# Optimization experiments

Hardware: AMD Instinct MI355X
Metric: run time of the kernel (lower is better)

The kernel has to match this reference:

```python
import jax, jax.numpy as jnp
import numpy as np

NPOINT = 1024
NSAMPLE = 32
RADIUS = 0.2


def index_points2(points, idx):
    # points: (B,N,D), idx: (B,S) -> (B,S,D)
    return jnp.take_along_axis(points, idx[..., None], axis=1)


def index_points3(points, idx):
    # points: (B,N,D), idx: (B,S,K) -> (B,S,K,D)
    B, S, K = idx.shape
    flat = jnp.take_along_axis(points, idx.reshape(B, S * K)[..., None], axis=1)
    return flat.reshape(B, S, K, points.shape[-1])


def farthest_point_sampling(xyz, npoint):
    # xyz: (B,N,3) -> (B,npoint) int32 indices. First point deterministic (index 0).
    B, N, _ = xyz.shape
    first = jnp.zeros((B,), jnp.int32)
    chosen = jnp.zeros((B, npoint), jnp.int32).at[:, 0].set(first)
    first_xyz = index_points2(xyz, first[:, None])[:, 0, :]
    dist_min = jnp.sum((xyz - first_xyz[:, None, :]) ** 2, axis=-1)  # (B,N)

    def body(i, carry):
        chosen, dist_min = carry
        far = jnp.argmax(dist_min, axis=-1).astype(jnp.int32)  # (B,)
        far_xyz = index_points2(xyz, far[:, None])[:, 0, :]
        d = jnp.sum((xyz - far_xyz[:, None, :]) ** 2, axis=-1)
        return chosen.at[:, i].set(far), jnp.minimum(dist_min, d)

    chosen, _ = jax.lax.fori_loop(1, npoint, body, (chosen, dist_min))
    return chosen


def query_ball_point(radius, nsample, xyz, new_xyz):
    # (B,S,N) squared distances; out-of-ball -> inf; take nsample nearest (stable argsort).
    dist = jnp.sum((new_xyz[:, :, None, :] - xyz[:, None, :, :]) ** 2, axis=-1)
    dist_m = jnp.where(dist <= radius ** 2, dist, jnp.inf)
    return jnp.argsort(dist_m, axis=-1)[:, :, :nsample]


def mlp2(x, Wa, ba, Wb, bb, act2):
    h = jax.nn.relu(x @ Wa + ba)
    return act2(h @ Wb + bb)


def reference(xyz, features, W1, b1, W2, b2, W3, b3, W4, b4):
    fps_idx = farthest_point_sampling(xyz, NPOINT)          # (B,S)
    new_xyz = index_points2(xyz, fps_idx)                   # (B,S,3)
    group_idx = query_ball_point(RADIUS, NSAMPLE, xyz, new_xyz)  # (B,S,K)
    grouped_xyz = index_points3(xyz, group_idx)             # (B,S,K,3)
    grouped_xyz_norm = grouped_xyz - new_xyz[:, :, None, :]
    grouped_feats = index_points3(features, group_idx)      # (B,S,K,C)
    f_in = jnp.concatenate([grouped_xyz_norm, grouped_feats], axis=-1)
    f_prime = mlp2(f_in, W1, b1, W2, b2, jax.nn.relu)       # (B,S,K,H)
    f_mean = jnp.mean(f_prime, axis=2, keepdims=True)
    w_in = jnp.concatenate([grouped_xyz_norm, f_prime - f_mean], axis=-1)
    alpha = mlp2(w_in, W3, b3, W4, b4, jax.nn.sigmoid)      # (B,S,K,H)
    f_out = jnp.sum(alpha * f_prime, axis=2)                # (B,S,H)
    return new_xyz, f_out


def setup_inputs() -> dict:
    key = jax.random.key(0)
    ks = jax.random.split(key, 8)
    B, N, C, H = 16, 4096, 64, 128
    xyz = jax.random.uniform(ks[0], (B, N, 3), dtype=jnp.float32)
    features = jax.random.normal(ks[1], (B, N, C), dtype=jnp.float32)
    s = 0.1
    return {
        "xyz": xyz,
        "features": features,
        "W1": jax.random.normal(ks[2], (3 + C, H), dtype=jnp.float32) * s,
        "b1": jnp.zeros((H,), jnp.float32),
        "W2": jax.random.normal(ks[3], (H, H), dtype=jnp.float32) * s,
        "b2": jnp.zeros((H,), jnp.float32),
        "W3": jax.random.normal(ks[4], (3 + H, H), dtype=jnp.float32) * s,
        "b3": jnp.zeros((H,), jnp.float32),
        "W4": jax.random.normal(ks[5], (H, H), dtype=jnp.float32) * s,
        "b4": jnp.zeros((H,), jnp.float32),
    }
```

## Files before the change

### kernel.cpp

```cpp
#include <hip/hip_runtime.h>

typedef unsigned short u16;
typedef unsigned int   u32;
typedef unsigned long long u64;
typedef short s8v __attribute__((ext_vector_type(8)));
typedef float f4v __attribute__((ext_vector_type(4)));
typedef float f2v __attribute__((ext_vector_type(2)));
typedef unsigned long long ull2 __attribute__((ext_vector_type(2)));

#define STRIDE 168
#define CAP 256
#define OFF_G1 0
#define OFF_G2 12288
#define OFF_G3 28672
#define OFF_G4 49152

__device__ __forceinline__ float bf2f(u16 u){ return __uint_as_float(((u32)u)<<16); }
__device__ __forceinline__ u16 f2bf(float f){
  u32 u = __float_as_uint(f);
  return (u16)((u + 0x7FFFu + ((u>>16)&1u)) >> 16);
}
__device__ __forceinline__ float sqd(float ax,float ay,float az,float bx,float by,float bz){
  float dx=ax-bx, dy=ay-by, dz=az-bz;
  return __fadd_rn(__fadd_rn(__fmul_rn(dx,dx),__fmul_rn(dy,dy)),__fmul_rn(dz,dz));
}

#define WMAX_STEP(v, CTRL) { \
  u32 _t = (u32)__builtin_amdgcn_update_dpp(0, (int)(v), CTRL, 0xf, 0xf, false); \
  (v) = (v) > _t ? (v) : _t; }
#define QMAX64(k, CTRL) { \
  u32 _lo=(u32)(k), _hi=(u32)((k)>>32); \
  u32 _plo=(u32)__builtin_amdgcn_update_dpp(0,(int)_lo,CTRL,0xf,0xf,true); \
  u32 _phi=(u32)__builtin_amdgcn_update_dpp(0,(int)_hi,CTRL,0xf,0xf,true); \
  u64 _o=((u64)_phi<<32)|_plo; (k) = (k)>_o ? (k) : _o; }

__global__ __launch_bounds__(512) void fps_kernel(const float* __restrict__ xyz,
                                                  float* __restrict__ newxyz){
  __shared__ __align__(16) float S[4096*3];
  __shared__ __align__(16) float R[1024*3];
  __shared__ u64 red[2][8];
  const int b = blockIdx.x, tid = threadIdx.x;
  const int lane = tid & 63, wv = tid >> 6;
  const float* xb = xyz + (size_t)b*4096*3;
  #pragma unroll
  for(int j=0;j<6;j++) ((float4*)S)[j*512+tid] = ((const float4*)xb)[j*512+tid];
  __syncthreads();
  f2v X[4],Y[4],Z[4],DM[4];
  const float x0=S[0], y0=S[1], z0=S[2];
  {
    #pragma clang fp contract(off)
    const f2v fx2={x0,x0}, fy2={y0,y0}, fz2={z0,z0};
    #pragma unroll
    for(int k2=0;k2<4;k2++){
      int p0 = tid*8 + 2*k2;
      X[k2] = (f2v){S[p0*3],   S[p0*3+3]};
      Y[k2] = (f2v){S[p0*3+1], S[p0*3+4]};
      Z[k2] = (f2v){S[p0*3+2], S[p0*3+5]};
      f2v dx=X[k2]-fx2, dy=Y[k2]-fy2, dz=Z[k2]-fz2;
      DM[k2] = (dx*dx + dy*dy) + dz*dz;
    }
  }
  if(tid==0){ R[0]=x0; R[1]=y0; R[2]=z0; }
  for(int i=1;i<1024;i++){
    f2v a = __builtin_elementwise_max(DM[0],DM[1]);
    f2v c = __builtin_elementwise_max(DM[2],DM[3]);
    f2v mm = __builtin_elementwise_max(a,c);
    float vm = fmaxf(mm[0], mm[1]);
    u32 m8 = 0;
    #pragma unroll
    for(int j=0;j<8;j++) m8 |= (DM[j>>1][j&1]==vm) ? (1u<<j) : 0u;
    int jm = __ffs(m8)-1;
    u32 w = __float_as_uint(vm);
    WMAX_STEP(w, 0x111); WMAX_STEP(w, 0x112); WMAX_STEP(w, 0x114);
    WMAX_STEP(w, 0x118); WMAX_STEP(w, 0x142); WMAX_STEP(w, 0x143);
    u32 wm = (u32)__builtin_amdgcn_readlane((int)w, 63);
    u64 msk = __ballot(__float_as_uint(vm) == wm);
    int ldr = __ffsll((unsigned long long)msk) - 1;
    int pj  = __builtin_amdgcn_readlane(jm, ldr);
    int p   = (wv*64 + ldr)*8 + pj;
    if(lane==0) red[i&1][wv] = ((u64)wm<<32) | (u32)(~(u32)p);
    __syncthreads();
    u64 k = red[i&1][lane&7];
    QMAX64(k, 0x121); QMAX64(k, 0x122); QMAX64(k, 0x124);
    int far = (int)(~(u32)k) & 4095;
    float fx=S[far*3], fy=S[far*3+1], fz=S[far*3+2];
    if(tid==0){ R[i*3]=fx; R[i*3+1]=fy; R[i*3+2]=fz; }
    {
      #pragma clang fp contract(off)
      const f2v fx2={fx,fx}, fy2={fy,fy}, fz2={fz,fz};
      #pragma unroll
      for(int k2c=0;k2c<4;k2c++){
        f2v dx=X[k2c]-fx2, dy=Y[k2c]-fy2, dz=Z[k2c]-fz2;
        f2v s = (dx*dx + dy*dy) + dz*dz;
        DM[k2c] = __builtin_elementwise_min(DM[k2c], s);
      }
    }
  }
  __syncthreads();
  float* nb = newxyz + (size_t)b*3072;
  if(tid<384){
    ((float4*)nb)[tid]     = ((const float4*)R)[tid];
    ((float4*)nb)[384+tid] = ((const float4*)R)[384+tid];
  }
}

__global__ __launch_bounds__(256) void ballq_kernel(const float* __restrict__ xyz,
                                                    const float* __restrict__ newxyz,
                                                    int* __restrict__ selg){
  __shared__ u64 Bc4[4][CAP+2];
  const int tid=threadIdx.x, wv=tid>>6, lane=tid&63;
  const int widx = blockIdx.x*4 + wv, b = widx>>10;
  const float* xb = xyz + (size_t)b*4096*3;
  const float cx=newxyz[widx*3], cy=newxyz[widx*3+1], cz=newxyz[widx*3+2];
  u64* Bc = Bc4[wv];
  int* selp = selg + (size_t)widx*128;
  const u64 lt = (1ull<<lane)-1ull;
  int base=0;
  for(int kk=0;kk<64;kk++){
    int p = kk*64 + lane;
    float d = sqd(cx,cy,cz, xb[p*3],xb[p*3+1],xb[p*3+2]);
    bool in = (d <= 0.04f);
    u64 m = __ballot(in);
    if(in){ int pos = base + __popcll(m&lt); if(pos<CAP) Bc[pos] = ((u64)__float_as_uint(d)<<32)|(u32)p; }
    base += __popcll(m);
  }
  int cnt = base>CAP ? CAP : base;
  if(cnt > 32){
    if(lane==0){ Bc[cnt]=~0ull; Bc[cnt+1]=~0ull; }
    int cnt2 = (cnt+1)&~1;
    for(int c=lane; c<cnt; c+=64){
      u64 key = Bc[c]; int r=0;
      for(int t2=0;t2<cnt2;t2+=2){
        ull2 k2 = *(const ull2*)&Bc[t2];
        r += (k2[0] < key) ? 1 : 0;
        r += (k2[1] < key) ? 1 : 0;
      }
      if(r < 32) selp[r] = (int)(u32)key;
    }
  } else {
    for(int c=lane; c<cnt; c+=64) selp[c] = (int)(u32)Bc[c];
    int need = 32 - cnt, b2 = 0;
    for(int kk=0; kk<64 && b2<need; kk++){
      int p = kk*64 + lane;
      float d = sqd(cx,cy,cz, xb[p*3],xb[p*3+1],xb[p*3+2]);
      bool o = !(d <= 0.04f);
      u64 m = __ballot(o);
      if(o){ int pos = b2 + __popcll(m&lt); if(pos<need) selp[cnt+pos] = p; }
      b2 += __popcll(m);
    }
  }
}

__global__ __launch_bounds__(256) void swz_kernel(const float* __restrict__ W1,const float* __restrict__ W2,
                                                  const float* __restrict__ W3,const float* __restrict__ W4,
                                                  u16* __restrict__ wsw){
  int T = blockIdx.x*256 + threadIdx.x;
  const float* W; int rel, base, kind;
  if(T < 1536){ rel=T;      base=OFF_G1; W=W1; kind=0; }
  else if(T < 3584){ rel=T-1536; base=OFF_G2; W=W2; kind=1; }
  else if(T < 6144){ rel=T-3584; base=OFF_G3; W=W3; kind=0; }
  else         { rel=T-6144; base=OFF_G4; W=W4; kind=1; }
  int chunk=rel>>6, lane=rel&63, c=chunk>>3, t=chunk&7, quad=lane>>4, l15=lane&15;
  u16 v[8];
  #pragma unroll
  for(int j=0;j<8;j++){
    int kp = c*32 + quad*8 + j, n = t*16 + l15;
    int src = (kind==0) ? (kp<3 ? kp : (kp>=32 ? kp-29 : -1)) : kp;
    v[j] = (src<0) ? (u16)0 : f2bf(W[src*128 + n]);
  }
  int4 o;
  o.x=(int)((u32)v[0]|((u32)v[1]<<16)); o.y=(int)((u32)v[2]|((u32)v[3]<<16));
  o.z=(int)((u32)v[4]|((u32)v[5]<<16)); o.w=(int)((u32)v[6]|((u32)v[7]<<16));
  *(int4*)&wsw[base + rel*8] = o;
}

__device__ __forceinline__ void zero_C(f4v C[2][8]){
  #pragma unroll
  for(int mt=0;mt<2;mt++)
    #pragma unroll
    for(int t=0;t<8;t++) C[mt][t] = (f4v){0.f,0.f,0.f,0.f};
}
__device__ __forceinline__ void load_bias(const float* bsrc,int l15,float bb[8]){
  #pragma unroll
  for(int t=0;t<8;t++) bb[t]=bsrc[t*16+l15];
}
template<int KC>
__device__ __forceinline__ void run_gemm(const u16* A, const u16* BW,
                                         int lane,int l15,int quad, f4v C[2][8]){
  s8v af[2][KC];
  #pragma unroll
  for(int mt=0;mt<2;mt++)
    #pragma unroll
    for(int c=0;c<KC;c++)
      af[mt][c] = *(const s8v*)&A[(mt*16+l15)*STRIDE + c*32 + quad*8];
  #pragma unroll
  for(int t=0;t<8;t++){
    #pragma unroll
    for(int c=0;c<KC;c++){
      s8v bw = *(const s8v*)&BW[((c*8+t)*64 + lane)*8];
      C[0][t] = __builtin_amdgcn_mfma_f32_16x16x32_bf16(af[0][c],bw,C[0][t],0,0,0);
      C[1][t] = __builtin_amdgcn_mfma_f32_16x16x32_bf16(af[1][c],bw,C[1][t],0,0,0);
    }
  }
}
__device__ __forceinline__ void store_act(u16* A,int l15,int quad,f4v C[2][8],const float bb[8]){
  #pragma unroll
  for(int mt=0;mt<2;mt++)
    #pragma unroll
    for(int t=0;t<8;t++)
      #pragma unroll
      for(int r=0;r<4;r++){
        float v = fmaxf(C[mt][t][r]+bb[t], 0.f);
        A[(mt*16+quad*4+r)*STRIDE + t*16 + l15] = f2bf(v);
      }
}
__device__ __forceinline__ void write_xyz_chunk0(u16* A,int lane,float xn,float yn,float zn){
  if(lane<32){
    u16* row=&A[lane*STRIDE];
    row[0]=f2bf(xn); row[1]=f2bf(yn); row[2]=f2bf(zn); row[3]=0;
    #pragma unroll
    for(int q=0;q<7;q++) *(u64*)&row[4+q*4] = 0ull;
  }
}

__global__ __launch_bounds__(256,3) void mlp_kernel(const float* __restrict__ xyz,
    const float* __restrict__ feats, const u16* __restrict__ wsw,
    const float* __restrict__ b1,const float* __restrict__ b2,const float* __restrict__ b3,const float* __restrict__ b4,
    const float* __restrict__ newxyz, float* __restrict__ fout){
  __shared__ __align__(16) u16 Abuf[4][32*STRIDE];
  const int tid=threadIdx.x, wv=tid>>6, lane=tid&63, quad=lane>>4, l15=lane&15;
  const int widx = blockIdx.x*4 + wv, b = widx>>10;
  u16* A = Abuf[wv];
  const float* xb = xyz + (size_t)b*4096*3;
  const float cx=newxyz[widx*3], cy=newxyz[widx*3+1], cz=newxyz[widx*3+2];
  const int* selp = (const int*)(fout + (size_t)widx*128);
  const int gi_f = selp[lane>>1] & 4095;
  const int gi_x = selp[lane & 31] & 4095;

  {
    int r2=lane>>1, h=lane&1;
    const float* fs = feats + ((size_t)b*4096 + gi_f)*64 + h*32;
    u16* fd = &A[r2*STRIDE + 32 + h*32];
    #pragma unroll
    for(int j=0;j<8;j++){
      float4 v4 = ((const float4*)fs)[j];
      u64 pk4 = (u64)f2bf(v4.x) | ((u64)f2bf(v4.y)<<16)
              | ((u64)f2bf(v4.z)<<32) | ((u64)f2bf(v4.w)<<48);
      *(u64*)&fd[j*4] = pk4;
    }
  }
  float xn=0.f,yn=0.f,zn=0.f;
  if(lane<32){
    const float* xp = xb + (size_t)gi_x*3;
    xn = xp[0]-cx; yn = xp[1]-cy; zn = xp[2]-cz;
  }
  write_xyz_chunk0(A,lane,xn,yn,zn);
  __syncthreads();

  f4v C[2][8]; float bb[8];
  zero_C(C); load_bias(b1,l15,bb);
  run_gemm<3>(A, wsw+OFF_G1, lane,l15,quad, C);
  store_act(A,l15,quad,C,bb);
  __syncthreads();
  zero_C(C); load_bias(b2,l15,bb);
  run_gemm<4>(A, wsw+OFF_G2, lane,l15,quad, C);
  float fp[2][8][4]; float mean[8];
  #pragma unroll
  for(int t=0;t<8;t++){
    float s=0.f;
    #pragma unroll
    for(int mt=0;mt<2;mt++)
      #pragma unroll
      for(int r=0;r<4;r++){
        float v = fmaxf(C[mt][t][r]+bb[t], 0.f);
        fp[mt][t][r]=v; s+=v;
      }
    s += __shfl_xor(s,16); s += __shfl_xor(s,32);
    mean[t] = s*0.03125f;
  }
  #pragma unroll
  for(int mt=0;mt<2;mt++)
    #pragma unroll
    for(int t=0;t<8;t++)
      #pragma unroll
      for(int r=0;r<4;r++)
        A[(mt*16+quad*4+r)*STRIDE + 32 + t*16 + l15] = f2bf(fp[mt][t][r]-mean[t]);
  write_xyz_chunk0(A,lane,xn,yn,zn);
  __syncthreads();
  zero_C(C); load_bias(b3,l15,bb);
  run_gemm<5>(A, wsw+OFF_G3, lane,l15,quad, C);
  store_act(A,l15,quad,C,bb);
  __syncthreads();
  zero_C(C); load_bias(b4,l15,bb);
  run_gemm<4>(A, wsw+OFF_G4, lane,l15,quad, C);
  float* fo = fout + (size_t)widx*128;
  #pragma unroll
  for(int t=0;t<8;t++){
    float part=0.f;
    #pragma unroll
    for(int mt=0;mt<2;mt++)
      #pragma unroll
      for(int r=0;r<4;r++){
        float pre = C[mt][t][r]+bb[t];
        float a = 1.f/(1.f+__expf(-pre));
        part += a*fp[mt][t][r];
      }
    part += __shfl_xor(part,16); part += __shfl_xor(part,32);
    if(quad==0) fo[t*16+l15] = part;
  }
}

extern "C" void kernel_launch(void* const* d_in, const int* in_sizes, int n_in,
                              void* d_out, int out_size, void* d_ws, size_t ws_size,
                              hipStream_t stream){
  (void)in_sizes; (void)n_in; (void)out_size; (void)ws_size;
  const float* xyz   = (const float*)d_in[0];
  const float* feats = (const float*)d_in[1];
  const float* W1 = (const float*)d_in[2]; const float* b1 = (const float*)d_in[3];
  const float* W2 = (const float*)d_in[4]; const float* b2 = (const float*)d_in[5];
  const float* W3 = (const float*)d_in[6]; const float* b3 = (const float*)d_in[7];
  const float* W4 = (const float*)d_in[8]; const float* b4 = (const float*)d_in[9];
  float* out = (float*)d_out;
  float* newxyz = out;
  float* fout   = out + 16*1024*3;
  u16* wsw = (u16*)d_ws;

  hipLaunchKernelGGL(swz_kernel,   dim3(32),   dim3(256), 0, stream, W1,W2,W3,W4, wsw);
  hipLaunchKernelGGL(fps_kernel,   dim3(16),   dim3(512), 0, stream, xyz, newxyz);
  hipLaunchKernelGGL(ballq_kernel, dim3(4096), dim3(256), 0, stream, xyz, newxyz, (int*)fout);
  hipLaunchKernelGGL(mlp_kernel,   dim3(4096), dim3(256), 0, stream,
                     xyz, feats, wsw, b1,b2,b3,b4, newxyz, fout);
}
```

Baseline: 968.5 us.

## Fuse FPS, ball query and MLP into persistent cooperative kernel with progress flags

Merges the separate FPS, ball-query and MLP kernels into one persistent cooperative kernel. The first 16 blocks run FPS and publish progress every 32 centroids through release-ordered global counters. The remaining waves take centroid tasks from an atomic ticket, spin-wait until that centroid is published, then run the ball query and MLP without intermediate global round trips or per-block syncs. This overlaps the long serial FPS phase with the downstream work. The cost is spin-wait polling, reliance on all blocks being co-resident, and a shared-memory union that caps occupancy.

```diff
diff --git a/kernel.cpp b/kernel.cpp
--- a/kernel.cpp
+++ b/kernel.cpp
@@ -14,8 +14,12 @@
 #define OFF_G2 12288
 #define OFF_G3 28672
 #define OFF_G4 49152
-
-__device__ __forceinline__ float bf2f(u16 u){ return __uint_as_float(((u32)u)<<16); }
+#define NTASK (16*1024)
+#define NBLK 240
+
+__device__ u32 g_prog[16];
+__device__ u32 g_ticket;
+
 __device__ __forceinline__ u16 f2bf(float f){
   u32 u = __float_as_uint(f);
   return (u16)((u + 0x7FFFu + ((u>>16)&1u)) >> 16);
@@ -33,123 +37,6 @@
   u32 _plo=(u32)__builtin_amdgcn_update_dpp(0,(int)_lo,CTRL,0xf,0xf,true); \
   u32 _phi=(u32)__builtin_amdgcn_update_dpp(0,(int)_hi,CTRL,0xf,0xf,true); \
   u64 _o=((u64)_phi<<32)|_plo; (k) = (k)>_o ? (k) : _o; }
-
-__global__ __launch_bounds__(512) void fps_kernel(const float* __restrict__ xyz,
-                                                  float* __restrict__ newxyz){
-  __shared__ __align__(16) float S[4096*3];
-  __shared__ __align__(16) float R[1024*3];
-  __shared__ u64 red[2][8];
-  const int b = blockIdx.x, tid = threadIdx.x;
-  const int lane = tid & 63, wv = tid >> 6;
-  const float* xb = xyz + (size_t)b*4096*3;
-  #pragma unroll
-  for(int j=0;j<6;j++) ((float4*)S)[j*512+tid] = ((const float4*)xb)[j*512+tid];
-  __syncthreads();
-  f2v X[4],Y[4],Z[4],DM[4];
-  const float x0=S[0], y0=S[1], z0=S[2];
-  {
-    #pragma clang fp contract(off)
-    const f2v fx2={x0,x0}, fy2={y0,y0}, fz2={z0,z0};
-    #pragma unroll
-    for(int k2=0;k2<4;k2++){
-      int p0 = tid*8 + 2*k2;
-      X[k2] = (f2v){S[p0*3],   S[p0*3+3]};
-      Y[k2] = (f2v){S[p0*3+1], S[p0*3+4]};
-      Z[k2] = (f2v){S[p0*3+2], S[p0*3+5]};
-      f2v dx=X[k2]-fx2, dy=Y[k2]-fy2, dz=Z[k2]-fz2;
-      DM[k2] = (dx*dx + dy*dy) + dz*dz;
-    }
-  }
-  if(tid==0){ R[0]=x0; R[1]=y0; R[2]=z0; }
-  for(int i=1;i<1024;i++){
-    f2v a = __builtin_elementwise_max(DM[0],DM[1]);
-    f2v c = __builtin_elementwise_max(DM[2],DM[3]);
-    f2v mm = __builtin_elementwise_max(a,c);
-    float vm = fmaxf(mm[0], mm[1]);
-    u32 m8 = 0;
-    #pragma unroll
-    for(int j=0;j<8;j++) m8 |= (DM[j>>1][j&1]==vm) ? (1u<<j) : 0u;
-    int jm = __ffs(m8)-1;
-    u32 w = __float_as_uint(vm);
-    WMAX_STEP(w, 0x111); WMAX_STEP(w, 0x112); WMAX_STEP(w, 0x114);
-    WMAX_STEP(w, 0x118); WMAX_STEP(w, 0x142); WMAX_STEP(w, 0x143);
-    u32 wm = (u32)__builtin_amdgcn_readlane((int)w, 63);
-    u64 msk = __ballot(__float_as_uint(vm) == wm);
-    int ldr = __ffsll((unsigned long long)msk) - 1;
-    int pj  = __builtin_amdgcn_readlane(jm, ldr);
-    int p   = (wv*64 + ldr)*8 + pj;
-    if(lane==0) red[i&1][wv] = ((u64)wm<<32) | (u32)(~(u32)p);
-    __syncthreads();
-    u64 k = red[i&1][lane&7];
-    QMAX64(k, 0x121); QMAX64(k, 0x122); QMAX64(k, 0x124);
-    int far = (int)(~(u32)k) & 4095;
-    float fx=S[far*3], fy=S[far*3+1], fz=S[far*3+2];
-    if(tid==0){ R[i*3]=fx; R[i*3+1]=fy; R[i*3+2]=fz; }
-    {
-      #pragma clang fp contract(off)
-      const f2v fx2={fx,fx}, fy2={fy,fy}, fz2={fz,fz};
-      #pragma unroll
-      for(int k2c=0;k2c<4;k2c++){
-        f2v dx=X[k2c]-fx2, dy=Y[k2c]-fy2, dz=Z[k2c]-fz2;
-        f2v s = (dx*dx + dy*dy) + dz*dz;
-        DM[k2c] = __builtin_elementwise_min(DM[k2c], s);
-      }
-    }
-  }
-  __syncthreads();
-  float* nb = newxyz + (size_t)b*3072;
-  if(tid<384){
-    ((float4*)nb)[tid]     = ((const float4*)R)[tid];
-    ((float4*)nb)[384+tid] = ((const float4*)R)[384+tid];
-  }
-}
-
-__global__ __launch_bounds__(256) void ballq_kernel(const float* __restrict__ xyz,
-                                                    const float* __restrict__ newxyz,
-                                                    int* __restrict__ selg){
-  __shared__ u64 Bc4[4][CAP+2];
-  const int tid=threadIdx.x, wv=tid>>6, lane=tid&63;
-  const int widx = blockIdx.x*4 + wv, b = widx>>10;
-  const float* xb = xyz + (size_t)b*4096*3;
-  const float cx=newxyz[widx*3], cy=newxyz[widx*3+1], cz=newxyz[widx*3+2];
-  u64* Bc = Bc4[wv];
-  int* selp = selg + (size_t)widx*128;
-  const u64 lt = (1ull<<lane)-1ull;
-  int base=0;
-  for(int kk=0;kk<64;kk++){
-    int p = kk*64 + lane;
-    float d = sqd(cx,cy,cz, xb[p*3],xb[p*3+1],xb[p*3+2]);
-    bool in = (d <= 0.04f);
-    u64 m = __ballot(in);
-    if(in){ int pos = base + __popcll(m&lt); if(pos<CAP) Bc[pos] = ((u64)__float_as_uint(d)<<32)|(u32)p; }
-    base += __popcll(m);
-  }
-  int cnt = base>CAP ? CAP : base;
-  if(cnt > 32){
-    if(lane==0){ Bc[cnt]=~0ull; Bc[cnt+1]=~0ull; }
-    int cnt2 = (cnt+1)&~1;
-    for(int c=lane; c<cnt; c+=64){
-      u64 key = Bc[c]; int r=0;
-      for(int t2=0;t2<cnt2;t2+=2){
-        ull2 k2 = *(const ull2*)&Bc[t2];
-        r += (k2[0] < key) ? 1 : 0;
-        r += (k2[1] < key) ? 1 : 0;
-      }
-      if(r < 32) selp[r] = (int)(u32)key;
-    }
-  } else {
-    for(int c=lane; c<cnt; c+=64) selp[c] = (int)(u32)Bc[c];
-    int need = 32 - cnt, b2 = 0;
-    for(int kk=0; kk<64 && b2<need; kk++){
-      int p = kk*64 + lane;
-      float d = sqd(cx,cy,cz, xb[p*3],xb[p*3+1],xb[p*3+2]);
-      bool o = !(d <= 0.04f);
-      u64 m = __ballot(o);
-      if(o){ int pos = b2 + __popcll(m&lt); if(pos<need) selp[cnt+pos] = p; }
-      b2 += __popcll(m);
-    }
-  }
-}
 
 __global__ __launch_bounds__(256) void swz_kernel(const float* __restrict__ W1,const float* __restrict__ W2,
                                                   const float* __restrict__ W3,const float* __restrict__ W4,
@@ -172,6 +59,11 @@
   o.x=(int)((u32)v[0]|((u32)v[1]<<16)); o.y=(int)((u32)v[2]|((u32)v[3]<<16));
   o.z=(int)((u32)v[4]|((u32)v[5]<<16)); o.w=(int)((u32)v[6]|((u32)v[7]<<16));
   *(int4*)&wsw[base + rel*8] = o;
+  if(T==0){
+    #pragma unroll
+    for(int i=0;i<16;i++) g_prog[i]=0;
+    g_ticket=0;
+  }
 }
 
 __device__ __forceinline__ void zero_C(f4v C[2][8]){
@@ -223,90 +115,206 @@
   }
 }
 
-__global__ __launch_bounds__(256,3) void mlp_kernel(const float* __restrict__ xyz,
+union SMem {
+  struct { float S[4096*3]; u64 red[2][8]; } f;
+  struct { u64 Bc[8][CAP+2]; int sel[8][32]; u16 A[8][32*STRIDE]; } c;
+};
+
+__global__ __launch_bounds__(512,2) void fused_kernel(const float* __restrict__ xyz,
     const float* __restrict__ feats, const u16* __restrict__ wsw,
-    const float* __restrict__ b1,const float* __restrict__ b2,const float* __restrict__ b3,const float* __restrict__ b4,
-    const float* __restrict__ newxyz, float* __restrict__ fout){
-  __shared__ __align__(16) u16 Abuf[4][32*STRIDE];
-  const int tid=threadIdx.x, wv=tid>>6, lane=tid&63, quad=lane>>4, l15=lane&15;
-  const int widx = blockIdx.x*4 + wv, b = widx>>10;
-  u16* A = Abuf[wv];
-  const float* xb = xyz + (size_t)b*4096*3;
-  const float cx=newxyz[widx*3], cy=newxyz[widx*3+1], cz=newxyz[widx*3+2];
-  const int* selp = (const int*)(fout + (size_t)widx*128);
-  const int gi_f = selp[lane>>1] & 4095;
-  const int gi_x = selp[lane & 31] & 4095;
-
-  {
-    int r2=lane>>1, h=lane&1;
-    const float* fs = feats + ((size_t)b*4096 + gi_f)*64 + h*32;
-    u16* fd = &A[r2*STRIDE + 32 + h*32];
-    #pragma unroll
-    for(int j=0;j<8;j++){
-      float4 v4 = ((const float4*)fs)[j];
-      u64 pk4 = (u64)f2bf(v4.x) | ((u64)f2bf(v4.y)<<16)
-              | ((u64)f2bf(v4.z)<<32) | ((u64)f2bf(v4.w)<<48);
-      *(u64*)&fd[j*4] = pk4;
-    }
-  }
-  float xn=0.f,yn=0.f,zn=0.f;
-  if(lane<32){
-    const float* xp = xb + (size_t)gi_x*3;
-    xn = xp[0]-cx; yn = xp[1]-cy; zn = xp[2]-cz;
-  }
-  write_xyz_chunk0(A,lane,xn,yn,zn);
+    const float* __restrict__ b1,const float* __restrict__ b2,
+    const float* __restrict__ b3,const float* __restrict__ b4,
+    float* __restrict__ newxyz, float* __restrict__ fout){
+  __shared__ __align__(16) SMem U;
+  const int tid=threadIdx.x, lane=tid&63, wv=tid>>6;
+
+  if(blockIdx.x < 16){
+    const int b = blockIdx.x;
+    float* S = U.f.S;
+    const float* xb = xyz + (size_t)b*4096*3;
+    #pragma unroll
+    for(int j=0;j<6;j++) ((float4*)S)[j*512+tid] = ((const float4*)xb)[j*512+tid];
+    __syncthreads();
+    f2v X[4],Y[4],Z[4],DM[4];
+    const float x0=S[0], y0=S[1], z0=S[2];
+    {
+      #pragma clang fp contract(off)
+      const f2v fx2={x0,x0}, fy2={y0,y0}, fz2={z0,z0};
+      #pragma unroll
+      for(int k2=0;k2<4;k2++){
+        int p0 = tid*8 + 2*k2;
+        X[k2] = (f2v){S[p0*3],   S[p0*3+3]};
+        Y[k2] = (f2v){S[p0*3+1], S[p0*3+4]};
+        Z[k2] = (f2v){S[p0*3+2], S[p0*3+5]};
+        f2v dx=X[k2]-fx2, dy=Y[k2]-fy2, dz=Z[k2]-fz2;
+        DM[k2] = (dx*dx + dy*dy) + dz*dz;
+      }
+    }
+    float* nb = newxyz + (size_t)b*3072;
+    if(tid==0){ nb[0]=x0; nb[1]=y0; nb[2]=z0; }
+    for(int i=1;i<1024;i++){
+      f2v a = __builtin_elementwise_max(DM[0],DM[1]);
+      f2v cc = __builtin_elementwise_max(DM[2],DM[3]);
+      f2v mm = __builtin_elementwise_max(a,cc);
+      float vm = fmaxf(mm[0], mm[1]);
+      u32 m8 = 0;
+      #pragma unroll
+      for(int j=0;j<8;j++) m8 |= (DM[j>>1][j&1]==vm) ? (1u<<j) : 0u;
+      int jm = __ffs(m8)-1;
+      u32 w = __float_as_uint(vm);
+      WMAX_STEP(w, 0x111); WMAX_STEP(w, 0x112); WMAX_STEP(w, 0x114);
+      WMAX_STEP(w, 0x118); WMAX_STEP(w, 0x142); WMAX_STEP(w, 0x143);
+      u32 wm = (u32)__builtin_amdgcn_readlane((int)w, 63);
+      u64 msk = __ballot(__float_as_uint(vm) == wm);
+      int ldr = __ffsll((unsigned long long)msk) - 1;
+      int pj  = __builtin_amdgcn_readlane(jm, ldr);
+      int p   = (wv*64 + ldr)*8 + pj;
+      if(lane==0) U.f.red[i&1][wv] = ((u64)wm<<32) | (u32)(~(u32)p);
+      __syncthreads();
+      u64 k = U.f.red[i&1][lane&7];
+      QMAX64(k, 0x121); QMAX64(k, 0x122); QMAX64(k, 0x124);
+      int far = (int)(~(u32)k) & 4095;
+      float fx=S[far*3], fy=S[far*3+1], fz=S[far*3+2];
+      if(tid==0){
+        float* r = nb + (size_t)i*3;
+        r[0]=fx; r[1]=fy; r[2]=fz;
+        if((i&31)==31)
+          __hip_atomic_store(&g_prog[b], (u32)(i+1), __ATOMIC_RELEASE, __HIP_MEMORY_SCOPE_AGENT);
+      }
+      {
+        #pragma clang fp contract(off)
+        const f2v fx2={fx,fx}, fy2={fy,fy}, fz2={fz,fz};
+        #pragma unroll
+        for(int k2c=0;k2c<4;k2c++){
+          f2v dx=X[k2c]-fx2, dy=Y[k2c]-fy2, dz=Z[k2c]-fz2;
+          f2v s2 = (dx*dx + dy*dy) + dz*dz;
+          DM[k2c] = __builtin_elementwise_min(DM[k2c], s2);
+        }
+      }
+    }
+  }
   __syncthreads();
 
-  f4v C[2][8]; float bb[8];
-  zero_C(C); load_bias(b1,l15,bb);
-  run_gemm<3>(A, wsw+OFF_G1, lane,l15,quad, C);
-  store_act(A,l15,quad,C,bb);
-  __syncthreads();
-  zero_C(C); load_bias(b2,l15,bb);
-  run_gemm<4>(A, wsw+OFF_G2, lane,l15,quad, C);
-  float fp[2][8][4]; float mean[8];
-  #pragma unroll
-  for(int t=0;t<8;t++){
-    float s=0.f;
+  const int quad=lane>>4, l15=lane&15;
+  u64* Bc   = U.c.Bc[wv];
+  int* selw = U.c.sel[wv];
+  u16* A    = U.c.A[wv];
+  const u64 lt = (1ull<<lane)-1ull;
+  for(;;){
+    int t;
+    if(lane==0) t = (int)atomicAdd(&g_ticket, 1u);
+    t = __shfl(t, 0);
+    if(t >= NTASK) break;
+    const int s = t>>4, tb = t&15, widx = (tb<<10) + s;
+    while(__hip_atomic_load(&g_prog[tb], __ATOMIC_ACQUIRE, __HIP_MEMORY_SCOPE_AGENT) <= (u32)s)
+      __builtin_amdgcn_s_sleep(8);
+    const float* xb = xyz + (size_t)tb*4096*3;
+    const float cx=newxyz[widx*3], cy=newxyz[widx*3+1], cz=newxyz[widx*3+2];
+
+    int base=0;
+    for(int kk=0;kk<64;kk++){
+      int p = kk*64 + lane;
+      float d = sqd(cx,cy,cz, xb[p*3],xb[p*3+1],xb[p*3+2]);
+      bool in = (d <= 0.04f);
+      u64 m = __ballot(in);
+      if(in){ int pos = base + __popcll(m&lt); if(pos<CAP) Bc[pos] = ((u64)__float_as_uint(d)<<32)|(u32)p; }
+      base += __popcll(m);
+    }
+    int cnt = base>CAP ? CAP : base;
+    if(cnt > 32){
+      if(lane==0){ Bc[cnt]=~0ull; Bc[cnt+1]=~0ull; }
+      int cnt2 = (cnt+1)&~1;
+      for(int c=lane; c<cnt; c+=64){
+        u64 key = Bc[c]; int r=0;
+        for(int t2=0;t2<cnt2;t2+=2){
+          ull2 k2 = *(const ull2*)&Bc[t2];
+          r += (k2[0] < key) ? 1 : 0;
+          r += (k2[1] < key) ? 1 : 0;
+        }
+        if(r < 32) selw[r] = (int)(u32)key;
+      }
+    } else {
+      for(int c=lane; c<cnt; c+=64) selw[c] = (int)(u32)Bc[c];
+      int need = 32 - cnt, bq = 0;
+      for(int kk=0; kk<64 && bq<need; kk++){
+        int p = kk*64 + lane;
+        float d = sqd(cx,cy,cz, xb[p*3],xb[p*3+1],xb[p*3+2]);
+        bool o = !(d <= 0.04f);
+        u64 m = __ballot(o);
+        if(o){ int pos = bq + __popcll(m&lt); if(pos<need) selw[cnt+pos] = p; }
+        bq += __popcll(m);
+      }
+    }
+
+    const int gi_f = selw[lane>>1] & 4095;
+    const int gi_x = selw[lane & 31] & 4095;
+    {
+      int r2=lane>>1, h=lane&1;
+      const float* fs = feats + ((size_t)tb*4096 + gi_f)*64 + h*32;
+      u16* fd = &A[r2*STRIDE + 32 + h*32];
+      #pragma unroll
+      for(int j=0;j<8;j++){
+        float4 v4 = ((const float4*)fs)[j];
+        u64 pk4 = (u64)f2bf(v4.x) | ((u64)f2bf(v4.y)<<16)
+                | ((u64)f2bf(v4.z)<<32) | ((u64)f2bf(v4.w)<<48);
+        *(u64*)&fd[j*4] = pk4;
+      }
+    }
+    float xn=0.f,yn=0.f,zn=0.f;
+    if(lane<32){
+      const float* xp = xb + (size_t)gi_x*3;
+      xn = xp[0]-cx; yn = xp[1]-cy; zn = xp[2]-cz;
+    }
+    write_xyz_chunk0(A,lane,xn,yn,zn);
+
+    f4v C[2][8]; float bb[8];
+    zero_C(C); load_bias(b1,l15,bb);
+    run_gemm<3>(A, wsw+OFF_G1, lane,l15,quad, C);
+    store_act(A,l15,quad,C,bb);
+    zero_C(C); load_bias(b2,l15,bb);
+    run_gemm<4>(A, wsw+OFF_G2, lane,l15,quad, C);
+    float fp[2][8][4]; float mean[8];
+    #pragma unroll
+    for(int t2=0;t2<8;t2++){
+      float sm=0.f;
+      #pragma unroll
+      for(int mt=0;mt<2;mt++)
+        #pragma unroll
+        for(int r=0;r<4;r++){
+          float v = fmaxf(C[mt][t2][r]+bb[t2], 0.f);
+          fp[mt][t2][r]=v; sm+=v;
+        }
+      sm += __shfl_xor(sm,16); sm += __shfl_xor(sm,32);
+      mean[t2] = sm*0.03125f;
+    }
     #pragma unroll
     for(int mt=0;mt<2;mt++)
       #pragma unroll
-      for(int r=0;r<4;r++){
-        float v = fmaxf(C[mt][t][r]+bb[t], 0.f);
-        fp[mt][t][r]=v; s+=v;
-      }
-    s += __shfl_xor(s,16); s += __shfl_xor(s,32);
-    mean[t] = s*0.03125f;
-  }
-  #pragma unroll
-  for(int mt=0;mt<2;mt++)
-    #pragma unroll
-    for(int t=0;t<8;t++)
-      #pragma unroll
-      for(int r=0;r<4;r++)
-        A[(mt*16+quad*4+r)*STRIDE + 32 + t*16 + l15] = f2bf(fp[mt][t][r]-mean[t]);
-  write_xyz_chunk0(A,lane,xn,yn,zn);
-  __syncthreads();
-  zero_C(C); load_bias(b3,l15,bb);
-  run_gemm<5>(A, wsw+OFF_G3, lane,l15,quad, C);
-  store_act(A,l15,quad,C,bb);
-  __syncthreads();
-  zero_C(C); load_bias(b4,l15,bb);
-  run_gemm<4>(A, wsw+OFF_G4, lane,l15,quad, C);
-  float* fo = fout + (size_t)widx*128;
-  #pragma unroll
-  for(int t=0;t<8;t++){
-    float part=0.f;
-    #pragma unroll
-    for(int mt=0;mt<2;mt++)
-      #pragma unroll
-      for(int r=0;r<4;r++){
-        float pre = C[mt][t][r]+bb[t];
-        float a = 1.f/(1.f+__expf(-pre));
-        part += a*fp[mt][t][r];
-      }
-    part += __shfl_xor(part,16); part += __shfl_xor(part,32);
-    if(quad==0) fo[t*16+l15] = part;
+      for(int t2=0;t2<8;t2++)
+        #pragma unroll
+        for(int r=0;r<4;r++)
+          A[(mt*16+quad*4+r)*STRIDE + 32 + t2*16 + l15] = f2bf(fp[mt][t2][r]-mean[t2]);
+    write_xyz_chunk0(A,lane,xn,yn,zn);
+    zero_C(C); load_bias(b3,l15,bb);
+    run_gemm<5>(A, wsw+OFF_G3, lane,l15,quad, C);
+    store_act(A,l15,quad,C,bb);
+    zero_C(C); load_bias(b4,l15,bb);
+    run_gemm<4>(A, wsw+OFF_G4, lane,l15,quad, C);
+    float* fo = fout + (size_t)widx*128;
+    #pragma unroll
+    for(int t2=0;t2<8;t2++){
+      float part=0.f;
+      #pragma unroll
+      for(int mt=0;mt<2;mt++)
+        #pragma unroll
+        for(int r=0;r<4;r++){
+          float pre = C[mt][t2][r]+bb[t2];
+          float aa = 1.f/(1.f+__expf(-pre));
+          part += aa*fp[mt][t2][r];
+        }
+      part += __shfl_xor(part,16); part += __shfl_xor(part,32);
+      if(quad==0) fo[t2*16+l15] = part;
+    }
   }
 }
 
@@ -325,9 +333,10 @@
   float* fout   = out + 16*1024*3;
   u16* wsw = (u16*)d_ws;
 
-  hipLaunchKernelGGL(swz_kernel,   dim3(32),   dim3(256), 0, stream, W1,W2,W3,W4, wsw);
-  hipLaunchKernelGGL(fps_kernel,   dim3(16),   dim3(512), 0, stream, xyz, newxyz);
-  hipLaunchKernelGGL(ballq_kernel, dim3(4096), dim3(256), 0, stream, xyz, newxyz, (int*)fout);
-  hipLaunchKernelGGL(mlp_kernel,   dim3(4096), dim3(256), 0, stream,
-                     xyz, feats, wsw, b1,b2,b3,b4, newxyz, fout);
-}
+  hipLaunchKernelGGL(swz_kernel, dim3(32), dim3(256), 0, stream, W1,W2,W3,W4, wsw);
+  void* args[9];
+  args[0]=(void*)&xyz;  args[1]=(void*)&feats; args[2]=(void*)&wsw;
+  args[3]=(void*)&b1;   args[4]=(void*)&b2;    args[5]=(void*)&b3; args[6]=(void*)&b4;
+  args[7]=(void*)&newxyz; args[8]=(void*)&fout;
+  hipLaunchCooperativeKernel((void*)fused_kernel, dim3(NBLK), dim3(512), args, 0, stream);
+}
```

Measured after the change: 1.183 ms. 22.2% more time.
